# Performance work log

Measured on AMD Instinct MI355X. Metric: run time of the kernel, lower is better.

The kernel has to match this reference:

```python
import jax, jax.numpy as jnp
import numpy as np

HIDDEN = 1024
OUT = 8192
N_SUBJ = 8
B = 64
T = 512


def setup_inputs() -> dict:
    key = jax.random.key(0)
    ks = jax.random.split(key, 12)
    s = 1.0 / np.sqrt(HIDDEN)
    return {
        "context": jax.random.normal(ks[0], (B, T, HIDDEN), dtype=jnp.float32),
        "subject_ids": jax.random.randint(ks[1], (B,), 0, N_SUBJ),
        "eps": jax.random.normal(ks[2], (B, OUT), dtype=jnp.float32),
        # pool_proj: Linear(H,H) -> GELU -> Linear(H,H); weights stored (in,out)
        "w1": jax.random.normal(ks[3], (HIDDEN, HIDDEN), dtype=jnp.float32) * s,
        "b1": jax.random.normal(ks[4], (HIDDEN,), dtype=jnp.float32) * s,
        "w2": jax.random.normal(ks[5], (HIDDEN, HIDDEN), dtype=jnp.float32) * s,
        "b2": jax.random.normal(ks[6], (HIDDEN,), dtype=jnp.float32) * s,
        # SubjectLayers params, init normal(0, 1/sqrt(in))
        "subj_w": jax.random.normal(ks[7], (N_SUBJ, HIDDEN, OUT), dtype=jnp.float32) * s,
        "subj_b": jax.random.normal(ks[8], (N_SUBJ, OUT), dtype=jnp.float32) * s,
        # log_var head: weight std 1e-4, bias -2.0
        "lv_w": jax.random.normal(ks[9], (HIDDEN, OUT), dtype=jnp.float32) * 1e-4,
        "lv_b": jnp.full((OUT,), -2.0, dtype=jnp.float32),
    }


def reference(context, subject_ids, eps, w1, b1, w2, b2, subj_w, subj_b, lv_w, lv_b):
    # mean-pool over time: (B,T,H) -> (B,H)
    h = context.mean(axis=1)
    # pool_proj MLP with exact GELU (torch default)
    h = jax.nn.gelu(h @ w1 + b1, approximate=False) @ w2 + b2
    # per-subject linear head: gather (H,OUT) weight per sample, matvec
    w = subj_w[subject_ids]            # (B, H, OUT)
    mu = jnp.einsum("bd,bdo->bo", h, w) + subj_b[subject_ids]
    # variational log-variance head, clamped
    log_var = jnp.clip(h @ lv_w + lv_b, -10.0, 2.0)
    # reparameterized sample (training mode)
    x0 = mu + eps * jnp.exp(0.5 * log_var)
    return x0, mu, log_var
```

## Files before the change

kernel.cpp:

```cpp
#include <hip/hip_runtime.h>
#include <math.h>

#define HID   1024
#define OUTD  8192
#define NSUBJ 8
#define BATCH 64
#define TLEN  512

#define OFF_PP    0u
#define OFF_P1    1048576u
#define OFF_P2    3145728u
#define OFF_H     5242880u
#define OFF_MUP   5308416u
#define OFF_LVP   9502720u

__global__ __launch_bounds__(256) void k_pool(const float* __restrict__ ctx,
                                              float* __restrict__ pp) {
    int b  = blockIdx.x;
    int tc = blockIdx.y;
    int hid = threadIdx.x * 4;
    const float* base = ctx + ((size_t)b * TLEN + (size_t)tc * 32) * HID + hid;
    float4 acc = make_float4(0.f, 0.f, 0.f, 0.f);
#pragma unroll 8
    for (int t = 0; t < 32; ++t) {
        float4 v = *(const float4*)(base + (size_t)t * HID);
        acc.x += v.x; acc.y += v.y; acc.z += v.z; acc.w += v.w;
    }
    *(float4*)(pp + ((size_t)tc * BATCH + b) * HID + hid) = acc;
}

__global__ __launch_bounds__(256) void k_mlp1(const float* __restrict__ pp,
                                              const float* __restrict__ w1,
                                              float* __restrict__ p1) {
    __shared__ float xs[32][34];
    int j  = blockIdx.x * 256 + threadIdx.x;
    int k0 = blockIdx.y * 32;
    int b0 = blockIdx.z * 32;
    {
        int bb = threadIdx.x >> 3;
        int kk = (threadIdx.x & 7) * 4;
        float4 s = make_float4(0.f, 0.f, 0.f, 0.f);
#pragma unroll
        for (int tc = 0; tc < 16; ++tc) {
            float4 v = *(const float4*)(pp + (size_t)tc * 65536 + (b0 + bb) * 1024 + k0 + kk);
            s.x += v.x; s.y += v.y; s.z += v.z; s.w += v.w;
        }
        const float inv = 1.0f / 512.0f;
        xs[bb][kk]     = s.x * inv;
        xs[bb][kk + 1] = s.y * inv;
        xs[bb][kk + 2] = s.z * inv;
        xs[bb][kk + 3] = s.w * inv;
    }
    __syncthreads();
    float acc[32];
#pragma unroll
    for (int i = 0; i < 32; ++i) acc[i] = 0.f;
    for (int kk = 0; kk < 32; kk += 2) {
        float wa = w1[(size_t)(k0 + kk) * HID + j];
        float wb = w1[(size_t)(k0 + kk + 1) * HID + j];
#pragma unroll
        for (int i = 0; i < 32; ++i) {
            acc[i] = fmaf(xs[i][kk], wa, acc[i]);
            acc[i] = fmaf(xs[i][kk + 1], wb, acc[i]);
        }
    }
    float* dst = p1 + (size_t)blockIdx.y * 65536;
#pragma unroll
    for (int i = 0; i < 32; ++i) dst[(b0 + i) * 1024 + j] = acc[i];
}

__global__ __launch_bounds__(256) void k_mlp2(const float* __restrict__ p1,
                                              const float* __restrict__ b1,
                                              const float* __restrict__ w2,
                                              float* __restrict__ p2) {
    __shared__ float xs[32][34];
    int j  = blockIdx.x * 256 + threadIdx.x;
    int k0 = blockIdx.y * 32;
    int b0 = blockIdx.z * 32;
    {
        int bb = threadIdx.x >> 3;
        int kk = (threadIdx.x & 7) * 4;
        float4 s = make_float4(0.f, 0.f, 0.f, 0.f);
#pragma unroll
        for (int kc = 0; kc < 32; ++kc) {
            float4 v = *(const float4*)(p1 + (size_t)kc * 65536 + (b0 + bb) * 1024 + k0 + kk);
            s.x += v.x; s.y += v.y; s.z += v.z; s.w += v.w;
        }
        float4 bbv = *(const float4*)(b1 + k0 + kk);
        s.x += bbv.x; s.y += bbv.y; s.z += bbv.z; s.w += bbv.w;
        const float r = 0.70710678118654752f;
        xs[bb][kk]     = 0.5f * s.x * (1.0f + erff(s.x * r));
        xs[bb][kk + 1] = 0.5f * s.y * (1.0f + erff(s.y * r));
        xs[bb][kk + 2] = 0.5f * s.z * (1.0f + erff(s.z * r));
        xs[bb][kk + 3] = 0.5f * s.w * (1.0f + erff(s.w * r));
    }
    __syncthreads();
    float acc[32];
#pragma unroll
    for (int i = 0; i < 32; ++i) acc[i] = 0.f;
    for (int kk = 0; kk < 32; kk += 2) {
        float wa = w2[(size_t)(k0 + kk) * HID + j];
        float wb = w2[(size_t)(k0 + kk + 1) * HID + j];
#pragma unroll
        for (int i = 0; i < 32; ++i) {
            acc[i] = fmaf(xs[i][kk], wa, acc[i]);
            acc[i] = fmaf(xs[i][kk + 1], wb, acc[i]);
        }
    }
    float* dst = p2 + (size_t)blockIdx.y * 65536;
#pragma unroll
    for (int i = 0; i < 32; ++i) dst[(b0 + i) * 1024 + j] = acc[i];
}

__global__ __launch_bounds__(256) void k_red_bias(const float* __restrict__ p,
                                                  const float* __restrict__ bias,
                                                  float* __restrict__ out) {
    int i = (blockIdx.x * 256 + threadIdx.x) * 4;
    int j = i & (HID - 1);
    float4 s = make_float4(0.f, 0.f, 0.f, 0.f);
#pragma unroll
    for (int kc = 0; kc < 32; ++kc) {
        float4 v = *(const float4*)(p + (size_t)kc * 65536 + i);
        s.x += v.x; s.y += v.y; s.z += v.z; s.w += v.w;
    }
    float4 bb = *(const float4*)(bias + j);
    s.x += bb.x; s.y += bb.y; s.z += bb.z; s.w += bb.w;
    *(float4*)(out + i) = s;
}

template <int NS>
__device__ __forceinline__ void mu_tile(const float* __restrict__ hmat,
                                        const float* __restrict__ wbase,
                                        float* __restrict__ mup_kc,
                                        const int* bo, int n, int k0, int o) {
    float4 acc[NS];
#pragma unroll
    for (int i = 0; i < NS; ++i) acc[i] = make_float4(0.f, 0.f, 0.f, 0.f);
    float4 wv[4];
#pragma unroll
    for (int kk = 0; kk < 4; ++kk)
        wv[kk] = *(const float4*)(wbase + (size_t)(k0 + kk) * OUTD + o);
    for (int k = k0; k < k0 + 128; k += 4) {
        float4 hv[NS];
#pragma unroll
        for (int i = 0; i < NS; ++i)
            hv[i] = *(const float4*)(hmat + bo[i] * HID + k);
        int kn = (k + 4 < k0 + 128) ? (k + 4) : k0;
        float4 wn[4];
#pragma unroll
        for (int kk = 0; kk < 4; ++kk)
            wn[kk] = *(const float4*)(wbase + (size_t)(kn + kk) * OUTD + o);
#pragma unroll
        for (int kk = 0; kk < 4; ++kk) {
            float4 w = wv[kk];
#pragma unroll
            for (int i = 0; i < NS; ++i) {
                float h = (kk == 0) ? hv[i].x : (kk == 1) ? hv[i].y
                        : (kk == 2) ? hv[i].z : hv[i].w;
                acc[i].x = fmaf(h, w.x, acc[i].x);
                acc[i].y = fmaf(h, w.y, acc[i].y);
                acc[i].z = fmaf(h, w.z, acc[i].z);
                acc[i].w = fmaf(h, w.w, acc[i].w);
            }
        }
#pragma unroll
        for (int kk = 0; kk < 4; ++kk) wv[kk] = wn[kk];
    }
#pragma unroll
    for (int i = 0; i < NS; ++i)
        if (i < n) *(float4*)(mup_kc + (size_t)bo[i] * OUTD + o) = acc[i];
}

__global__ __launch_bounds__(256) void k_mu(const float* __restrict__ hmat,
                                            const float* __restrict__ subj_w,
                                            const int* __restrict__ sid,
                                            float* __restrict__ mup) {
    int o  = blockIdx.x * 1024 + threadIdx.x * 4;
    int k0 = blockIdx.y * 128;
    int s  = blockIdx.z;
    int lane = threadIdx.x & 63;
    int mysid = sid[lane];
    unsigned long long m = __ballot(mysid == s);
    int ns = __popcll(m);
    if (ns == 0) return;
    const float* wbase = subj_w + (size_t)s * HID * OUTD;
    float* mup_kc = mup + (size_t)blockIdx.y * BATCH * OUTD;
    unsigned long long mm = m;
    for (int base = 0; base < ns; base += 12) {
        int take = ns - base; if (take > 12) take = 12;
        int fb = (int)__builtin_ctzll(mm);
        int bo[12];
#pragma unroll
        for (int i = 0; i < 12; ++i) {
            bo[i] = (mm != 0ull) ? (int)__builtin_ctzll(mm) : fb;
            if (mm != 0ull) mm &= (mm - 1ull);
        }
        if (take <= 4)       mu_tile<4>(hmat, wbase, mup_kc, bo, take, k0, o);
        else if (take <= 8)  mu_tile<8>(hmat, wbase, mup_kc, bo, take, k0, o);
        else                 mu_tile<12>(hmat, wbase, mup_kc, bo, take, k0, o);
    }
}

__global__ __launch_bounds__(256) void k_lv(const float* __restrict__ hmat,
                                            const float* __restrict__ lv_w,
                                            float* __restrict__ lvp) {
    int o  = blockIdx.x * 512 + threadIdx.x * 2;
    int k0 = blockIdx.y * 128;
    int b0 = blockIdx.z * 32;
    float2 acc[32];
#pragma unroll
    for (int i = 0; i < 32; ++i) acc[i] = make_float2(0.f, 0.f);
    float2 wv0 = *(const float2*)(lv_w + (size_t)k0 * OUTD + o);
    float2 wv1 = *(const float2*)(lv_w + (size_t)(k0 + 1) * OUTD + o);
    for (int k = k0; k < k0 + 128; k += 2) {
        float2 hv[32];
#pragma unroll
        for (int i = 0; i < 32; ++i)
            hv[i] = *(const float2*)(hmat + (b0 + i) * HID + k);
        int kn = (k + 2 < k0 + 128) ? (k + 2) : k0;
        float2 wn0 = *(const float2*)(lv_w + (size_t)kn * OUTD + o);
        float2 wn1 = *(const float2*)(lv_w + (size_t)(kn + 1) * OUTD + o);
#pragma unroll
        for (int i = 0; i < 32; ++i) {
            acc[i].x = fmaf(hv[i].x, wv0.x, acc[i].x);
            acc[i].y = fmaf(hv[i].x, wv0.y, acc[i].y);
            acc[i].x = fmaf(hv[i].y, wv1.x, acc[i].x);
            acc[i].y = fmaf(hv[i].y, wv1.y, acc[i].y);
        }
        wv0 = wn0; wv1 = wn1;
    }
#pragma unroll
    for (int i = 0; i < 32; ++i) {
        float* dst = lvp + ((size_t)blockIdx.y * BATCH + b0 + i) * OUTD + o;
        dst[0] = acc[i].x; dst[1] = acc[i].y;
    }
}

__global__ __launch_bounds__(256) void k_combine(const float* __restrict__ mup,
                                                 const float* __restrict__ lvp,
                                                 const float* __restrict__ eps,
                                                 const float* __restrict__ subj_b,
                                                 const float* __restrict__ lv_b,
                                                 const int* __restrict__ sid,
                                                 float* __restrict__ out) {
    int idx = (blockIdx.x * 256 + threadIdx.x) * 4;
    int b = idx >> 13;
    int o = idx & (OUTD - 1);
    float4 m = make_float4(0.f, 0.f, 0.f, 0.f);
    float4 l = make_float4(0.f, 0.f, 0.f, 0.f);
#pragma unroll
    for (int kc = 0; kc < 8; ++kc) {
        float4 t = *(const float4*)(mup + (size_t)kc * 524288 + idx);
        m.x += t.x; m.y += t.y; m.z += t.z; m.w += t.w;
        float4 u = *(const float4*)(lvp + (size_t)kc * 524288 + idx);
        l.x += u.x; l.y += u.y; l.z += u.z; l.w += u.w;
    }
    int s = sid[b];
    float4 sb = *(const float4*)(subj_b + s * OUTD + o);
    float4 lb = *(const float4*)(lv_b + o);
    m.x += sb.x; m.y += sb.y; m.z += sb.z; m.w += sb.w;
    l.x = fminf(fmaxf(l.x + lb.x, -10.f), 2.f);
    l.y = fminf(fmaxf(l.y + lb.y, -10.f), 2.f);
    l.z = fminf(fmaxf(l.z + lb.z, -10.f), 2.f);
    l.w = fminf(fmaxf(l.w + lb.w, -10.f), 2.f);
    float4 e = *(const float4*)(eps + idx);
    float4 x0;
    x0.x = m.x + e.x * __expf(0.5f * l.x);
    x0.y = m.y + e.y * __expf(0.5f * l.y);
    x0.z = m.z + e.z * __expf(0.5f * l.z);
    x0.w = m.w + e.w * __expf(0.5f * l.w);
    *(float4*)(out + idx) = x0;
    *(float4*)(out + 524288 + idx) = m;
    *(float4*)(out + 1048576 + idx) = l;
}

extern "C" void kernel_launch(void* const* d_in, const int* in_sizes, int n_in,
                              void* d_out, int out_size, void* d_ws, size_t ws_size,
                              hipStream_t stream) {
    const float* ctx    = (const float*)d_in[0];
    const int*   sid    = (const int*)  d_in[1];
    const float* eps    = (const float*)d_in[2];
    const float* w1     = (const float*)d_in[3];
    const float* b1     = (const float*)d_in[4];
    const float* w2     = (const float*)d_in[5];
    const float* b2     = (const float*)d_in[6];
    const float* subj_w = (const float*)d_in[7];
    const float* subj_b = (const float*)d_in[8];
    const float* lv_w   = (const float*)d_in[9];
    const float* lv_b   = (const float*)d_in[10];
    float* out = (float*)d_out;

    float* ws   = (float*)d_ws;
    float* pp   = ws + OFF_PP;
    float* p1   = ws + OFF_P1;
    float* p2   = ws + OFF_P2;
    float* hbuf = ws + OFF_H;
    float* mup  = ws + OFF_MUP;
    float* lvp  = ws + OFF_LVP;

    k_pool<<<dim3(BATCH, 16), 256, 0, stream>>>(ctx, pp);
    k_mlp1<<<dim3(4, 32, 2), 256, 0, stream>>>(pp, w1, p1);
    k_mlp2<<<dim3(4, 32, 2), 256, 0, stream>>>(p1, b1, w2, p2);
    k_red_bias<<<64, 256, 0, stream>>>(p2, b2, hbuf);
    k_mu<<<dim3(8, 8, NSUBJ), 256, 0, stream>>>(hbuf, subj_w, sid, mup);
    k_lv<<<dim3(16, 8, 2), 256, 0, stream>>>(hbuf, lv_w, lvp);
    k_combine<<<512, 256, 0, stream>>>(mup, lvp, eps, subj_b, lv_b, sid, out);
}
```

Baseline: 184.6 us.

## Fuse all stages into one cooperative persistent kernel with grid syncs

New measurement: 556.7 us. 202% more time.

```diff
diff --git a/kernel.cpp b/kernel.cpp
--- a/kernel.cpp
+++ b/kernel.cpp
@@ -1,5 +1,8 @@
 #include <hip/hip_runtime.h>
+#include <hip/hip_cooperative_groups.h>
 #include <math.h>
+
+namespace cg = cooperative_groups;
 
 #define HID   1024
 #define OUTD  8192
@@ -9,10 +12,315 @@
 
 #define OFF_PP    0u
 #define OFF_P1    1048576u
-#define OFF_P2    3145728u
-#define OFF_H     5242880u
-#define OFF_MUP   5308416u
-#define OFF_LVP   9502720u
+#define OFF_P2    2097152u
+#define OFF_H     3145728u
+#define OFF_MUP   3211264u
+#define OFF_LVP   7405568u
+#define OFF_CNT   11599872u
+
+template <int NS>
+__device__ __forceinline__ void mu_tile(const float* __restrict__ hmat,
+                                        const float* __restrict__ wbase,
+                                        float* __restrict__ mup_kc,
+                                        const int* bo, int n, int k0, int o) {
+    float4 acc[NS];
+#pragma unroll
+    for (int i = 0; i < NS; ++i) acc[i] = make_float4(0.f, 0.f, 0.f, 0.f);
+    float4 wv[4];
+#pragma unroll
+    for (int kk = 0; kk < 4; ++kk)
+        wv[kk] = *(const float4*)(wbase + (size_t)(k0 + kk) * OUTD + o);
+    for (int k = k0; k < k0 + 128; k += 4) {
+        float4 hv[NS];
+#pragma unroll
+        for (int i = 0; i < NS; ++i)
+            hv[i] = *(const float4*)(hmat + bo[i] * HID + k);
+        int kn = (k + 4 < k0 + 128) ? (k + 4) : k0;
+        float4 wn[4];
+#pragma unroll
+        for (int kk = 0; kk < 4; ++kk)
+            wn[kk] = *(const float4*)(wbase + (size_t)(kn + kk) * OUTD + o);
+#pragma unroll
+        for (int kk = 0; kk < 4; ++kk) {
+            float4 w = wv[kk];
+#pragma unroll
+            for (int i = 0; i < NS; ++i) {
+                float h = (kk == 0) ? hv[i].x : (kk == 1) ? hv[i].y
+                        : (kk == 2) ? hv[i].z : hv[i].w;
+                acc[i].x = fmaf(h, w.x, acc[i].x);
+                acc[i].y = fmaf(h, w.y, acc[i].y);
+                acc[i].z = fmaf(h, w.z, acc[i].z);
+                acc[i].w = fmaf(h, w.w, acc[i].w);
+            }
+        }
+#pragma unroll
+        for (int kk = 0; kk < 4; ++kk) wv[kk] = wn[kk];
+    }
+#pragma unroll
+    for (int i = 0; i < NS; ++i)
+        if (i < n) *(float4*)(mup_kc + (size_t)bo[i] * OUTD + o) = acc[i];
+}
+
+__device__ __forceinline__ void mu_task(int t, const float* __restrict__ hbuf,
+                                        const float* __restrict__ subj_w,
+                                        const int* __restrict__ sid,
+                                        float* __restrict__ mup, int tid) {
+    int o  = (t >> 6) * 1024 + tid * 4;
+    int kc = (t >> 3) & 7;
+    int s  = t & 7;
+    int k0 = kc * 128;
+    int lane = tid & 63;
+    int mysid = sid[lane];
+    unsigned long long m = __ballot(mysid == s);
+    int ns = __popcll(m);
+    if (ns == 0) return;
+    const float* wbase = subj_w + (size_t)s * HID * OUTD;
+    float* mup_kc = mup + (size_t)kc * BATCH * OUTD;
+    unsigned long long mm = m;
+    for (int base = 0; base < ns; base += 12) {
+        int take = ns - base; if (take > 12) take = 12;
+        int fb = (int)__builtin_ctzll(mm);
+        int bo[12];
+#pragma unroll
+        for (int i = 0; i < 12; ++i) {
+            bo[i] = (mm != 0ull) ? (int)__builtin_ctzll(mm) : fb;
+            if (mm != 0ull) mm &= (mm - 1ull);
+        }
+        if (take <= 4)       mu_tile<4>(hbuf, wbase, mup_kc, bo, take, k0, o);
+        else if (take <= 8)  mu_tile<8>(hbuf, wbase, mup_kc, bo, take, k0, o);
+        else                 mu_tile<12>(hbuf, wbase, mup_kc, bo, take, k0, o);
+    }
+}
+
+__device__ __forceinline__ void lv_task(int u, const float* __restrict__ hbuf,
+                                        const float* __restrict__ lv_w,
+                                        float* __restrict__ lvp, int tid) {
+    int o  = (u & 15) * 512 + tid * 2;
+    int kc = (u >> 4) & 7;
+    int b0 = (u >> 7) * 32;
+    int k0 = kc * 128;
+    float2 acc[32];
+#pragma unroll
+    for (int i = 0; i < 32; ++i) acc[i] = make_float2(0.f, 0.f);
+    float2 wv0 = *(const float2*)(lv_w + (size_t)k0 * OUTD + o);
+    float2 wv1 = *(const float2*)(lv_w + (size_t)(k0 + 1) * OUTD + o);
+    for (int k = k0; k < k0 + 128; k += 2) {
+        float2 hv[32];
+#pragma unroll
+        for (int i = 0; i < 32; ++i)
+            hv[i] = *(const float2*)(hbuf + (b0 + i) * HID + k);
+        int kn = (k + 2 < k0 + 128) ? (k + 2) : k0;
+        float2 wn0 = *(const float2*)(lv_w + (size_t)kn * OUTD + o);
+        float2 wn1 = *(const float2*)(lv_w + (size_t)(kn + 1) * OUTD + o);
+#pragma unroll
+        for (int i = 0; i < 32; ++i) {
+            acc[i].x = fmaf(hv[i].x, wv0.x, acc[i].x);
+            acc[i].y = fmaf(hv[i].x, wv0.y, acc[i].y);
+            acc[i].x = fmaf(hv[i].y, wv1.x, acc[i].x);
+            acc[i].y = fmaf(hv[i].y, wv1.y, acc[i].y);
+        }
+        wv0 = wn0; wv1 = wn1;
+    }
+#pragma unroll
+    for (int i = 0; i < 32; ++i) {
+        float* dst = lvp + ((size_t)kc * BATCH + b0 + i) * OUTD + o;
+        dst[0] = acc[i].x; dst[1] = acc[i].y;
+    }
+}
+
+__global__ __launch_bounds__(256, 2) void k_fused(
+        const float* __restrict__ ctx, const int* __restrict__ sid,
+        const float* __restrict__ eps,
+        const float* __restrict__ w1, const float* __restrict__ b1,
+        const float* __restrict__ w2, const float* __restrict__ b2,
+        const float* __restrict__ subj_w, const float* __restrict__ subj_b,
+        const float* __restrict__ lv_w, const float* __restrict__ lv_b,
+        float* __restrict__ out, float* __restrict__ ws) {
+    cg::grid_group grid = cg::this_grid();
+    float* pp   = ws + OFF_PP;
+    float* p1   = ws + OFF_P1;
+    float* p2   = ws + OFF_P2;
+    float* hbuf = ws + OFF_H;
+    float* mup  = ws + OFF_MUP;
+    float* lvp  = ws + OFF_LVP;
+    int* counter = (int*)(ws + OFF_CNT);
+    const int bid = blockIdx.x;
+    const int nb  = gridDim.x;
+    const int tid = threadIdx.x;
+    __shared__ float xs[32][72];
+    __shared__ int task_s;
+
+    if (bid == 0 && tid == 0) *counter = 0;
+    for (int t = bid; t < 1024; t += nb) {
+        int b = t >> 4, tc = t & 15;
+        int hid = tid * 4;
+        const float* base = ctx + ((size_t)b * TLEN + (size_t)tc * 32) * HID + hid;
+        float4 acc = make_float4(0.f, 0.f, 0.f, 0.f);
+#pragma unroll 8
+        for (int tt = 0; tt < 32; ++tt) {
+            float4 v = *(const float4*)(base + (size_t)tt * HID);
+            acc.x += v.x; acc.y += v.y; acc.z += v.z; acc.w += v.w;
+        }
+        *(float4*)(pp + ((size_t)tc * BATCH + b) * HID + hid) = acc;
+    }
+    __threadfence();
+    grid.sync();
+
+    for (int t = bid; t < 128; t += nb) {
+        int j  = (t & 3) * 256 + tid;
+        int k0 = ((t >> 2) & 15) * 64;
+        int b0 = (t >> 6) * 32;
+        {
+            int bb = tid >> 3;
+            int kk8 = (tid & 7) * 8;
+            float4 s0 = make_float4(0.f, 0.f, 0.f, 0.f);
+            float4 s1 = make_float4(0.f, 0.f, 0.f, 0.f);
+#pragma unroll
+            for (int tc = 0; tc < 16; ++tc) {
+                const float* bp = pp + (size_t)tc * 65536 + (b0 + bb) * HID + k0 + kk8;
+                float4 v0 = *(const float4*)bp;
+                float4 v1 = *(const float4*)(bp + 4);
+                s0.x += v0.x; s0.y += v0.y; s0.z += v0.z; s0.w += v0.w;
+                s1.x += v1.x; s1.y += v1.y; s1.z += v1.z; s1.w += v1.w;
+            }
+            const float inv = 1.0f / 512.0f;
+            s0.x *= inv; s0.y *= inv; s0.z *= inv; s0.w *= inv;
+            s1.x *= inv; s1.y *= inv; s1.z *= inv; s1.w *= inv;
+            *(float4*)&xs[bb][kk8]     = s0;
+            *(float4*)&xs[bb][kk8 + 4] = s1;
+        }
+        __syncthreads();
+        float acc[32];
+#pragma unroll
+        for (int i = 0; i < 32; ++i) acc[i] = 0.f;
+        for (int kk = 0; kk < 64; kk += 2) {
+            float wa = w1[(size_t)(k0 + kk) * HID + j];
+            float wb = w1[(size_t)(k0 + kk + 1) * HID + j];
+#pragma unroll
+            for (int i = 0; i < 32; ++i) {
+                acc[i] = fmaf(xs[i][kk], wa, acc[i]);
+                acc[i] = fmaf(xs[i][kk + 1], wb, acc[i]);
+            }
+        }
+        float* dst = p1 + (size_t)((t >> 2) & 15) * 65536;
+#pragma unroll
+        for (int i = 0; i < 32; ++i) dst[(b0 + i) * HID + j] = acc[i];
+        __syncthreads();
+    }
+    __threadfence();
+    grid.sync();
+
+    for (int t = bid; t < 128; t += nb) {
+        int j  = (t & 3) * 256 + tid;
+        int k0 = ((t >> 2) & 15) * 64;
+        int b0 = (t >> 6) * 32;
+        {
+            int bb = tid >> 3;
+            int kk8 = (tid & 7) * 8;
+            float4 s0 = make_float4(0.f, 0.f, 0.f, 0.f);
+            float4 s1 = make_float4(0.f, 0.f, 0.f, 0.f);
+#pragma unroll
+            for (int kc = 0; kc < 16; ++kc) {
+                const float* bp = p1 + (size_t)kc * 65536 + (b0 + bb) * HID + k0 + kk8;
+                float4 v0 = *(const float4*)bp;
+                float4 v1 = *(const float4*)(bp + 4);
+                s0.x += v0.x; s0.y += v0.y; s0.z += v0.z; s0.w += v0.w;
+                s1.x += v1.x; s1.y += v1.y; s1.z += v1.z; s1.w += v1.w;
+            }
+            float4 bv0 = *(const float4*)(b1 + k0 + kk8);
+            float4 bv1 = *(const float4*)(b1 + k0 + kk8 + 4);
+            s0.x += bv0.x; s0.y += bv0.y; s0.z += bv0.z; s0.w += bv0.w;
+            s1.x += bv1.x; s1.y += bv1.y; s1.z += bv1.z; s1.w += bv1.w;
+            const float r = 0.70710678118654752f;
+            xs[bb][kk8]     = 0.5f * s0.x * (1.0f + erff(s0.x * r));
+            xs[bb][kk8 + 1] = 0.5f * s0.y * (1.0f + erff(s0.y * r));
+            xs[bb][kk8 + 2] = 0.5f * s0.z * (1.0f + erff(s0.z * r));
+            xs[bb][kk8 + 3] = 0.5f * s0.w * (1.0f + erff(s0.w * r));
+            xs[bb][kk8 + 4] = 0.5f * s1.x * (1.0f + erff(s1.x * r));
+            xs[bb][kk8 + 5] = 0.5f * s1.y * (1.0f + erff(s1.y * r));
+            xs[bb][kk8 + 6] = 0.5f * s1.z * (1.0f + erff(s1.z * r));
+            xs[bb][kk8 + 7] = 0.5f * s1.w * (1.0f + erff(s1.w * r));
+        }
+        __syncthreads();
+        float acc[32];
+#pragma unroll
+        for (int i = 0; i < 32; ++i) acc[i] = 0.f;
+        for (int kk = 0; kk < 64; kk += 2) {
+            float wa = w2[(size_t)(k0 + kk) * HID + j];
+            float wb = w2[(size_t)(k0 + kk + 1) * HID + j];
+#pragma unroll
+            for (int i = 0; i < 32; ++i) {
+                acc[i] = fmaf(xs[i][kk], wa, acc[i]);
+                acc[i] = fmaf(xs[i][kk + 1], wb, acc[i]);
+            }
+        }
+        float* dst = p2 + (size_t)((t >> 2) & 15) * 65536;
+#pragma unroll
+        for (int i = 0; i < 32; ++i) dst[(b0 + i) * HID + j] = acc[i];
+        __syncthreads();
+    }
+    __threadfence();
+    grid.sync();
+
+    for (int t = bid; t < 64; t += nb) {
+        int i = t * 1024 + tid * 4;
+        float4 s = make_float4(0.f, 0.f, 0.f, 0.f);
+#pragma unroll
+        for (int kc = 0; kc < 16; ++kc) {
+            float4 v = *(const float4*)(p2 + (size_t)kc * 65536 + i);
+            s.x += v.x; s.y += v.y; s.z += v.z; s.w += v.w;
+        }
+        float4 bb = *(const float4*)(b2 + tid * 4);
+        s.x += bb.x; s.y += bb.y; s.z += bb.z; s.w += bb.w;
+        *(float4*)(hbuf + i) = s;
+    }
+    __threadfence();
+    grid.sync();
+
+    for (;;) {
+        __syncthreads();
+        if (tid == 0) task_s = atomicAdd(counter, 1);
+        __syncthreads();
+        int t = task_s;
+        if (t >= 768) break;
+        if (t < 512) mu_task(t, hbuf, subj_w, sid, mup, tid);
+        else         lv_task(t - 512, hbuf, lv_w, lvp, tid);
+    }
+    __threadfence();
+    grid.sync();
+
+    for (int t = bid; t < 512; t += nb) {
+        int idx = t * 1024 + tid * 4;
+        int b = idx >> 13;
+        int o = idx & (OUTD - 1);
+        float4 m = make_float4(0.f, 0.f, 0.f, 0.f);
+        float4 l = make_float4(0.f, 0.f, 0.f, 0.f);
+#pragma unroll
+        for (int kc = 0; kc < 8; ++kc) {
+            float4 tv = *(const float4*)(mup + (size_t)kc * 524288 + idx);
+            m.x += tv.x; m.y += tv.y; m.z += tv.z; m.w += tv.w;
+            float4 u = *(const float4*)(lvp + (size_t)kc * 524288 + idx);
+            l.x += u.x; l.y += u.y; l.z += u.z; l.w += u.w;
+        }
+        int s = sid[b];
+        float4 sb = *(const float4*)(subj_b + s * OUTD + o);
+        float4 lb = *(const float4*)(lv_b + o);
+        m.x += sb.x; m.y += sb.y; m.z += sb.z; m.w += sb.w;
+        l.x = fminf(fmaxf(l.x + lb.x, -10.f), 2.f);
+        l.y = fminf(fmaxf(l.y + lb.y, -10.f), 2.f);
+        l.z = fminf(fmaxf(l.z + lb.z, -10.f), 2.f);
+        l.w = fminf(fmaxf(l.w + lb.w, -10.f), 2.f);
+        float4 e = *(const float4*)(eps + idx);
+        float4 x0;
+        x0.x = m.x + e.x * __expf(0.5f * l.x);
+        x0.y = m.y + e.y * __expf(0.5f * l.y);
+        x0.z = m.z + e.z * __expf(0.5f * l.z);
+        x0.w = m.w + e.w * __expf(0.5f * l.w);
+        *(float4*)(out + idx) = x0;
+        *(float4*)(out + 524288 + idx) = m;
+        *(float4*)(out + 1048576 + idx) = l;
+    }
+}
 
 __global__ __launch_bounds__(256) void k_pool(const float* __restrict__ ctx,
                                               float* __restrict__ pp) {
@@ -114,126 +422,36 @@
 
 __global__ __launch_bounds__(256) void k_red_bias(const float* __restrict__ p,
                                                   const float* __restrict__ bias,
-                                                  float* __restrict__ out) {
+                                                  float* __restrict__ out,
+                                                  int nchunk) {
     int i = (blockIdx.x * 256 + threadIdx.x) * 4;
     int j = i & (HID - 1);
     float4 s = make_float4(0.f, 0.f, 0.f, 0.f);
-#pragma unroll
-    for (int kc = 0; kc < 32; ++kc) {
+    for (int kc = 0; kc < nchunk; ++kc) {
         float4 v = *(const float4*)(p + (size_t)kc * 65536 + i);
         s.x += v.x; s.y += v.y; s.z += v.z; s.w += v.w;
     }
     float4 bb = *(const float4*)(bias + j);
     s.x += bb.x; s.y += bb.y; s.z += bb.z; s.w += bb.w;
     *(float4*)(out + i) = s;
-}
-
-template <int NS>
-__device__ __forceinline__ void mu_tile(const float* __restrict__ hmat,
-                                        const float* __restrict__ wbase,
-                                        float* __restrict__ mup_kc,
-                                        const int* bo, int n, int k0, int o) {
-    float4 acc[NS];
-#pragma unroll
-    for (int i = 0; i < NS; ++i) acc[i] = make_float4(0.f, 0.f, 0.f, 0.f);
-    float4 wv[4];
-#pragma unroll
-    for (int kk = 0; kk < 4; ++kk)
-        wv[kk] = *(const float4*)(wbase + (size_t)(k0 + kk) * OUTD + o);
-    for (int k = k0; k < k0 + 128; k += 4) {
-        float4 hv[NS];
-#pragma unroll
-        for (int i = 0; i < NS; ++i)
-            hv[i] = *(const float4*)(hmat + bo[i] * HID + k);
-        int kn = (k + 4 < k0 + 128) ? (k + 4) : k0;
-        float4 wn[4];
-#pragma unroll
-        for (int kk = 0; kk < 4; ++kk)
-            wn[kk] = *(const float4*)(wbase + (size_t)(kn + kk) * OUTD + o);
-#pragma unroll
-        for (int kk = 0; kk < 4; ++kk) {
-            float4 w = wv[kk];
-#pragma unroll
-            for (int i = 0; i < NS; ++i) {
-                float h = (kk == 0) ? hv[i].x : (kk == 1) ? hv[i].y
-                        : (kk == 2) ? hv[i].z : hv[i].w;
-                acc[i].x = fmaf(h, w.x, acc[i].x);
-                acc[i].y = fmaf(h, w.y, acc[i].y);
-                acc[i].z = fmaf(h, w.z, acc[i].z);
-                acc[i].w = fmaf(h, w.w, acc[i].w);
-            }
-        }
-#pragma unroll
-        for (int kk = 0; kk < 4; ++kk) wv[kk] = wn[kk];
-    }
-#pragma unroll
-    for (int i = 0; i < NS; ++i)
-        if (i < n) *(float4*)(mup_kc + (size_t)bo[i] * OUTD + o) = acc[i];
 }
 
 __global__ __launch_bounds__(256) void k_mu(const float* __restrict__ hmat,
                                             const float* __restrict__ subj_w,
                                             const int* __restrict__ sid,
                                             float* __restrict__ mup) {
-    int o  = blockIdx.x * 1024 + threadIdx.x * 4;
-    int k0 = blockIdx.y * 128;
-    int s  = blockIdx.z;
-    int lane = threadIdx.x & 63;
-    int mysid = sid[lane];
-    unsigned long long m = __ballot(mysid == s);
-    int ns = __popcll(m);
-    if (ns == 0) return;
-    const float* wbase = subj_w + (size_t)s * HID * OUTD;
-    float* mup_kc = mup + (size_t)blockIdx.y * BATCH * OUTD;
-    unsigned long long mm = m;
-    for (int base = 0; base < ns; base += 12) {
-        int take = ns - base; if (take > 12) take = 12;
-        int fb = (int)__builtin_ctzll(mm);
-        int bo[12];
-#pragma unroll
-        for (int i = 0; i < 12; ++i) {
-            bo[i] = (mm != 0ull) ? (int)__builtin_ctzll(mm) : fb;
-            if (mm != 0ull) mm &= (mm - 1ull);
-        }
-        if (take <= 4)       mu_tile<4>(hmat, wbase, mup_kc, bo, take, k0, o);
-        else if (take <= 8)  mu_tile<8>(hmat, wbase, mup_kc, bo, take, k0, o);
-        else                 mu_tile<12>(hmat, wbase, mup_kc, bo, take, k0, o);
-    }
+    int t = (blockIdx.z * 8 + blockIdx.y) * 8 + blockIdx.x;
+    (void)t;
+    int tid = threadIdx.x;
+    int task = ((blockIdx.x) << 6) + (blockIdx.y << 3) + blockIdx.z;
+    mu_task(task, hmat, subj_w, sid, mup, tid);
 }
 
 __global__ __launch_bounds__(256) void k_lv(const float* __restrict__ hmat,
                                             const float* __restrict__ lv_w,
                                             float* __restrict__ lvp) {
-    int o  = blockIdx.x * 512 + threadIdx.x * 2;
-    int k0 = blockIdx.y * 128;
-    int b0 = blockIdx.z * 32;
-    float2 acc[32];
-#pragma unroll
-    for (int i = 0; i < 32; ++i) acc[i] = make_float2(0.f, 0.f);
-    float2 wv0 = *(const float2*)(lv_w + (size_t)k0 * OUTD + o);
-    float2 wv1 = *(const float2*)(lv_w + (size_t)(k0 + 1) * OUTD + o);
-    for (int k = k0; k < k0 + 128; k += 2) {
-        float2 hv[32];
-#pragma unroll
-        for (int i = 0; i < 32; ++i)
-            hv[i] = *(const float2*)(hmat + (b0 + i) * HID + k);
-        int kn = (k + 2 < k0 + 128) ? (k + 2) : k0;
-        float2 wn0 = *(const float2*)(lv_w + (size_t)kn * OUTD + o);
-        float2 wn1 = *(const float2*)(lv_w + (size_t)(kn + 1) * OUTD + o);
-#pragma unroll
-        for (int i = 0; i < 32; ++i) {
-            acc[i].x = fmaf(hv[i].x, wv0.x, acc[i].x);
-            acc[i].y = fmaf(hv[i].x, wv0.y, acc[i].y);
-            acc[i].x = fmaf(hv[i].y, wv1.x, acc[i].x);
-            acc[i].y = fmaf(hv[i].y, wv1.y, acc[i].y);
-        }
-        wv0 = wn0; wv1 = wn1;
-    }
-#pragma unroll
-    for (int i = 0; i < 32; ++i) {
-        float* dst = lvp + ((size_t)blockIdx.y * BATCH + b0 + i) * OUTD + o;
-        dst[0] = acc[i].x; dst[1] = acc[i].y;
-    }
+    int u = (blockIdx.z << 7) + (blockIdx.y << 4) + blockIdx.x;
+    lv_task(u, hmat, lv_w, lvp, threadIdx.x);
 }
 
 __global__ __launch_bounds__(256) void k_combine(const float* __restrict__ mup,
@@ -289,8 +507,8 @@
     const float* lv_w   = (const float*)d_in[9];
     const float* lv_b   = (const float*)d_in[10];
     float* out = (float*)d_out;
-
-    float* ws   = (float*)d_ws;
+    float* ws  = (float*)d_ws;
+
     float* pp   = ws + OFF_PP;
     float* p1   = ws + OFF_P1;
     float* p2   = ws + OFF_P2;
@@ -298,10 +516,30 @@
     float* mup  = ws + OFF_MUP;
     float* lvp  = ws + OFF_LVP;
 
+    int dev = 0;
+    (void)hipGetDevice(&dev);
+    int coop = 0;
+    (void)hipDeviceGetAttribute(&coop, hipDeviceAttributeCooperativeLaunch, dev);
+    int occ = 0;
+    (void)hipOccupancyMaxActiveBlocksPerMultiprocessor(&occ, (const void*)k_fused, 256, 0);
+
+    if (coop && occ >= 1) {
+        int blocks = (occ >= 2) ? 512 : 256;
+        void* args[] = {
+            (void*)&ctx, (void*)&sid, (void*)&eps,
+            (void*)&w1, (void*)&b1, (void*)&w2, (void*)&b2,
+            (void*)&subj_w, (void*)&subj_b, (void*)&lv_w, (void*)&lv_b,
+            (void*)&out, (void*)&ws
+        };
+        hipError_t err = hipLaunchCooperativeKernel((const void*)k_fused, dim3(blocks),
+                                                    dim3(256), args, 0, stream);
+        if (err == hipSuccess) return;
+    }
+
     k_pool<<<dim3(BATCH, 16), 256, 0, stream>>>(ctx, pp);
     k_mlp1<<<dim3(4, 32, 2), 256, 0, stream>>>(pp, w1, p1);
     k_mlp2<<<dim3(4, 32, 2), 256, 0, stream>>>(p1, b1, w2, p2);
-    k_red_bias<<<64, 256, 0, stream>>>(p2, b2, hbuf);
+    k_red_bias<<<64, 256, 0, stream>>>(p2, b2, hbuf, 16);
     k_mu<<<dim3(8, 8, NSUBJ), 256, 0, stream>>>(hbuf, subj_w, sid, mup);
     k_lv<<<dim3(16, 8, 2), 256, 0, stream>>>(hbuf, lv_w, lvp);
     k_combine<<<512, 256, 0, stream>>>(mup, lvp, eps, subj_b, lv_b, sid, out);
```

## Fuse mu and log-var heads into one launch, split K finer for more blocks

Applied to the files above, without the earlier changes.

After: 207.8 us. +12.6%, slower.

```diff
diff --git a/kernel.cpp b/kernel.cpp
--- a/kernel.cpp
+++ b/kernel.cpp
@@ -8,21 +8,21 @@
 #define TLEN  512
 
 #define OFF_PP    0u
-#define OFF_P1    1048576u
-#define OFF_P2    3145728u
-#define OFF_H     5242880u
-#define OFF_MUP   5308416u
-#define OFF_LVP   9502720u
+#define OFF_P1    2097152u
+#define OFF_P2    4194304u
+#define OFF_H     6291456u
+#define OFF_MUP   6356992u
+#define OFF_LVP   14745600u
 
 __global__ __launch_bounds__(256) void k_pool(const float* __restrict__ ctx,
                                               float* __restrict__ pp) {
     int b  = blockIdx.x;
     int tc = blockIdx.y;
     int hid = threadIdx.x * 4;
-    const float* base = ctx + ((size_t)b * TLEN + (size_t)tc * 32) * HID + hid;
+    const float* base = ctx + ((size_t)b * TLEN + (size_t)tc * 16) * HID + hid;
     float4 acc = make_float4(0.f, 0.f, 0.f, 0.f);
-#pragma unroll 8
-    for (int t = 0; t < 32; ++t) {
+#pragma unroll
+    for (int t = 0; t < 16; ++t) {
         float4 v = *(const float4*)(base + (size_t)t * HID);
         acc.x += v.x; acc.y += v.y; acc.z += v.z; acc.w += v.w;
     }
@@ -41,7 +41,7 @@
         int kk = (threadIdx.x & 7) * 4;
         float4 s = make_float4(0.f, 0.f, 0.f, 0.f);
 #pragma unroll
-        for (int tc = 0; tc < 16; ++tc) {
+        for (int tc = 0; tc < 32; ++tc) {
             float4 v = *(const float4*)(pp + (size_t)tc * 65536 + (b0 + bb) * 1024 + k0 + kk);
             s.x += v.x; s.y += v.y; s.z += v.z; s.w += v.w;
         }
@@ -140,12 +140,12 @@
 #pragma unroll
     for (int kk = 0; kk < 4; ++kk)
         wv[kk] = *(const float4*)(wbase + (size_t)(k0 + kk) * OUTD + o);
-    for (int k = k0; k < k0 + 128; k += 4) {
+    for (int k = k0; k < k0 + 64; k += 4) {
         float4 hv[NS];
 #pragma unroll
         for (int i = 0; i < NS; ++i)
             hv[i] = *(const float4*)(hmat + bo[i] * HID + k);
-        int kn = (k + 4 < k0 + 128) ? (k + 4) : k0;
+        int kn = (k + 4 < k0 + 64) ? (k + 4) : k0;
         float4 wn[4];
 #pragma unroll
         for (int kk = 0; kk < 4; ++kk)
@@ -171,68 +171,73 @@
         if (i < n) *(float4*)(mup_kc + (size_t)bo[i] * OUTD + o) = acc[i];
 }
 
-__global__ __launch_bounds__(256) void k_mu(const float* __restrict__ hmat,
-                                            const float* __restrict__ subj_w,
-                                            const int* __restrict__ sid,
-                                            float* __restrict__ mup) {
-    int o  = blockIdx.x * 1024 + threadIdx.x * 4;
-    int k0 = blockIdx.y * 128;
-    int s  = blockIdx.z;
-    int lane = threadIdx.x & 63;
-    int mysid = sid[lane];
-    unsigned long long m = __ballot(mysid == s);
-    int ns = __popcll(m);
-    if (ns == 0) return;
-    const float* wbase = subj_w + (size_t)s * HID * OUTD;
-    float* mup_kc = mup + (size_t)blockIdx.y * BATCH * OUTD;
-    unsigned long long mm = m;
-    for (int base = 0; base < ns; base += 12) {
-        int take = ns - base; if (take > 12) take = 12;
-        int fb = (int)__builtin_ctzll(mm);
-        int bo[12];
-#pragma unroll
-        for (int i = 0; i < 12; ++i) {
-            bo[i] = (mm != 0ull) ? (int)__builtin_ctzll(mm) : fb;
-            if (mm != 0ull) mm &= (mm - 1ull);
-        }
-        if (take <= 4)       mu_tile<4>(hmat, wbase, mup_kc, bo, take, k0, o);
-        else if (take <= 8)  mu_tile<8>(hmat, wbase, mup_kc, bo, take, k0, o);
-        else                 mu_tile<12>(hmat, wbase, mup_kc, bo, take, k0, o);
-    }
-}
-
-__global__ __launch_bounds__(256) void k_lv(const float* __restrict__ hmat,
-                                            const float* __restrict__ lv_w,
-                                            float* __restrict__ lvp) {
-    int o  = blockIdx.x * 512 + threadIdx.x * 2;
-    int k0 = blockIdx.y * 128;
-    int b0 = blockIdx.z * 32;
-    float2 acc[32];
-#pragma unroll
-    for (int i = 0; i < 32; ++i) acc[i] = make_float2(0.f, 0.f);
-    float2 wv0 = *(const float2*)(lv_w + (size_t)k0 * OUTD + o);
-    float2 wv1 = *(const float2*)(lv_w + (size_t)(k0 + 1) * OUTD + o);
-    for (int k = k0; k < k0 + 128; k += 2) {
-        float2 hv[32];
-#pragma unroll
-        for (int i = 0; i < 32; ++i)
-            hv[i] = *(const float2*)(hmat + (b0 + i) * HID + k);
-        int kn = (k + 2 < k0 + 128) ? (k + 2) : k0;
-        float2 wn0 = *(const float2*)(lv_w + (size_t)kn * OUTD + o);
-        float2 wn1 = *(const float2*)(lv_w + (size_t)(kn + 1) * OUTD + o);
+__global__ __launch_bounds__(256) void k_head(const float* __restrict__ hbuf,
+                                              const float* __restrict__ subj_w,
+                                              const float* __restrict__ lv_w,
+                                              const int* __restrict__ sid,
+                                              float* __restrict__ mup,
+                                              float* __restrict__ lvp) {
+    int blk = blockIdx.x;
+    int tid = threadIdx.x;
+    if (blk < 1024) {
+        int o  = (blk >> 7) * 1024 + tid * 4;
+        int kc = (blk >> 3) & 15;
+        int s  = blk & 7;
+        int k0 = kc * 64;
+        int lane = tid & 63;
+        int mysid = sid[lane];
+        unsigned long long m = __ballot(mysid == s);
+        int ns = __popcll(m);
+        if (ns == 0) return;
+        const float* wbase = subj_w + (size_t)s * HID * OUTD;
+        float* mup_kc = mup + (size_t)kc * BATCH * OUTD;
+        unsigned long long mm = m;
+        for (int base = 0; base < ns; base += 12) {
+            int take = ns - base; if (take > 12) take = 12;
+            int fb = (int)__builtin_ctzll(mm);
+            int bo[12];
+#pragma unroll
+            for (int i = 0; i < 12; ++i) {
+                bo[i] = (mm != 0ull) ? (int)__builtin_ctzll(mm) : fb;
+                if (mm != 0ull) mm &= (mm - 1ull);
+            }
+            if (take <= 4)       mu_tile<4>(hbuf, wbase, mup_kc, bo, take, k0, o);
+            else if (take <= 8)  mu_tile<8>(hbuf, wbase, mup_kc, bo, take, k0, o);
+            else                 mu_tile<12>(hbuf, wbase, mup_kc, bo, take, k0, o);
+        }
+    } else {
+        int u  = blk - 1024;
+        int o  = (u & 15) * 512 + tid * 2;
+        int kc = (u >> 4) & 7;
+        int b0 = (u >> 7) * 32;
+        int k0 = kc * 128;
+        float2 acc[32];
+#pragma unroll
+        for (int i = 0; i < 32; ++i) acc[i] = make_float2(0.f, 0.f);
+        float2 wv0 = *(const float2*)(lv_w + (size_t)k0 * OUTD + o);
+        float2 wv1 = *(const float2*)(lv_w + (size_t)(k0 + 1) * OUTD + o);
+        for (int k = k0; k < k0 + 128; k += 2) {
+            float2 hv[32];
+#pragma unroll
+            for (int i = 0; i < 32; ++i)
+                hv[i] = *(const float2*)(hbuf + (b0 + i) * HID + k);
+            int kn = (k + 2 < k0 + 128) ? (k + 2) : k0;
+            float2 wn0 = *(const float2*)(lv_w + (size_t)kn * OUTD + o);
+            float2 wn1 = *(const float2*)(lv_w + (size_t)(kn + 1) * OUTD + o);
+#pragma unroll
+            for (int i = 0; i < 32; ++i) {
+                acc[i].x = fmaf(hv[i].x, wv0.x, acc[i].x);
+                acc[i].y = fmaf(hv[i].x, wv0.y, acc[i].y);
+                acc[i].x = fmaf(hv[i].y, wv1.x, acc[i].x);
+                acc[i].y = fmaf(hv[i].y, wv1.y, acc[i].y);
+            }
+            wv0 = wn0; wv1 = wn1;
+        }
 #pragma unroll
         for (int i = 0; i < 32; ++i) {
-            acc[i].x = fmaf(hv[i].x, wv0.x, acc[i].x);
-            acc[i].y = fmaf(hv[i].x, wv0.y, acc[i].y);
-            acc[i].x = fmaf(hv[i].y, wv1.x, acc[i].x);
-            acc[i].y = fmaf(hv[i].y, wv1.y, acc[i].y);
-        }
-        wv0 = wn0; wv1 = wn1;
-    }
-#pragma unroll
-    for (int i = 0; i < 32; ++i) {
-        float* dst = lvp + ((size_t)blockIdx.y * BATCH + b0 + i) * OUTD + o;
-        dst[0] = acc[i].x; dst[1] = acc[i].y;
+            float* dst = lvp + ((size_t)kc * BATCH + b0 + i) * OUTD + o;
+            dst[0] = acc[i].x; dst[1] = acc[i].y;
+        }
     }
 }
 
@@ -249,9 +254,12 @@
     float4 m = make_float4(0.f, 0.f, 0.f, 0.f);
     float4 l = make_float4(0.f, 0.f, 0.f, 0.f);
 #pragma unroll
-    for (int kc = 0; kc < 8; ++kc) {
+    for (int kc = 0; kc < 16; ++kc) {
         float4 t = *(const float4*)(mup + (size_t)kc * 524288 + idx);
         m.x += t.x; m.y += t.y; m.z += t.z; m.w += t.w;
+    }
+#pragma unroll
+    for (int kc = 0; kc < 8; ++kc) {
         float4 u = *(const float4*)(lvp + (size_t)kc * 524288 + idx);
         l.x += u.x; l.y += u.y; l.z += u.z; l.w += u.w;
     }
@@ -298,11 +306,10 @@
     float* mup  = ws + OFF_MUP;
     float* lvp  = ws + OFF_LVP;
 
-    k_pool<<<dim3(BATCH, 16), 256, 0, stream>>>(ctx, pp);
+    k_pool<<<dim3(BATCH, 32), 256, 0, stream>>>(ctx, pp);
     k_mlp1<<<dim3(4, 32, 2), 256, 0, stream>>>(pp, w1, p1);
     k_mlp2<<<dim3(4, 32, 2), 256, 0, stream>>>(p1, b1, w2, p2);
     k_red_bias<<<64, 256, 0, stream>>>(p2, b2, hbuf);
-    k_mu<<<dim3(8, 8, NSUBJ), 256, 0, stream>>>(hbuf, subj_w, sid, mup);
-    k_lv<<<dim3(16, 8, 2), 256, 0, stream>>>(hbuf, lv_w, lvp);
+    k_head<<<1280, 256, 0, stream>>>(hbuf, subj_w, lv_w, sid, mup, lvp);
     k_combine<<<512, 256, 0, stream>>>(mup, lvp, eps, subj_b, lv_b, sid, out);
 }
```

## Retile log-var head GEMM with shared-memory h and finer K split

Applied to the files above, without the earlier changes.

Measured after the change: 177.8 us. 1.04x faster.

```diff
diff --git a/kernel.cpp b/kernel.cpp
--- a/kernel.cpp
+++ b/kernel.cpp
@@ -204,36 +204,42 @@
 __global__ __launch_bounds__(256) void k_lv(const float* __restrict__ hmat,
                                             const float* __restrict__ lv_w,
                                             float* __restrict__ lvp) {
-    int o  = blockIdx.x * 512 + threadIdx.x * 2;
-    int k0 = blockIdx.y * 128;
-    int b0 = blockIdx.z * 32;
-    float2 acc[32];
-#pragma unroll
-    for (int i = 0; i < 32; ++i) acc[i] = make_float2(0.f, 0.f);
-    float2 wv0 = *(const float2*)(lv_w + (size_t)k0 * OUTD + o);
-    float2 wv1 = *(const float2*)(lv_w + (size_t)(k0 + 1) * OUTD + o);
-    for (int k = k0; k < k0 + 128; k += 2) {
-        float2 hv[32];
-#pragma unroll
-        for (int i = 0; i < 32; ++i)
-            hv[i] = *(const float2*)(hmat + (b0 + i) * HID + k);
-        int kn = (k + 2 < k0 + 128) ? (k + 2) : k0;
-        float2 wn0 = *(const float2*)(lv_w + (size_t)kn * OUTD + o);
-        float2 wn1 = *(const float2*)(lv_w + (size_t)(kn + 1) * OUTD + o);
-#pragma unroll
-        for (int i = 0; i < 32; ++i) {
-            acc[i].x = fmaf(hv[i].x, wv0.x, acc[i].x);
-            acc[i].y = fmaf(hv[i].x, wv0.y, acc[i].y);
-            acc[i].x = fmaf(hv[i].y, wv1.x, acc[i].x);
-            acc[i].y = fmaf(hv[i].y, wv1.y, acc[i].y);
-        }
-        wv0 = wn0; wv1 = wn1;
-    }
-#pragma unroll
-    for (int i = 0; i < 32; ++i) {
-        float* dst = lvp + ((size_t)blockIdx.y * BATCH + b0 + i) * OUTD + o;
-        dst[0] = acc[i].x; dst[1] = acc[i].y;
-    }
+    __shared__ float hs[64][20];
+    int o  = blockIdx.x * 1024 + threadIdx.x * 4;
+    int k0 = blockIdx.y * 64;
+    int b0 = blockIdx.z * 16;
+    {
+        int k  = threadIdx.x & 63;
+        int s4 = threadIdx.x >> 6;
+#pragma unroll
+        for (int j = 0; j < 4; ++j)
+            hs[k][s4 * 4 + j] = hmat[(size_t)(b0 + s4 * 4 + j) * HID + k0 + k];
+    }
+    __syncthreads();
+    float4 acc[16];
+#pragma unroll
+    for (int i = 0; i < 16; ++i) acc[i] = make_float4(0.f, 0.f, 0.f, 0.f);
+    const float* wp = lv_w + (size_t)k0 * OUTD + o;
+#pragma unroll 4
+    for (int k = 0; k < 64; ++k) {
+        float4 w = *(const float4*)(wp + (size_t)k * OUTD);
+        float4 h0 = *(const float4*)&hs[k][0];
+        float4 h1 = *(const float4*)&hs[k][4];
+        float4 h2 = *(const float4*)&hs[k][8];
+        float4 h3 = *(const float4*)&hs[k][12];
+        float hv[16] = {h0.x, h0.y, h0.z, h0.w, h1.x, h1.y, h1.z, h1.w,
+                        h2.x, h2.y, h2.z, h2.w, h3.x, h3.y, h3.z, h3.w};
+#pragma unroll
+        for (int i = 0; i < 16; ++i) {
+            acc[i].x = fmaf(hv[i], w.x, acc[i].x);
+            acc[i].y = fmaf(hv[i], w.y, acc[i].y);
+            acc[i].z = fmaf(hv[i], w.z, acc[i].z);
+            acc[i].w = fmaf(hv[i], w.w, acc[i].w);
+        }
+    }
+#pragma unroll
+    for (int i = 0; i < 16; ++i)
+        *(float4*)(lvp + ((size_t)blockIdx.y * BATCH + b0 + i) * OUTD + o) = acc[i];
 }
 
 __global__ __launch_bounds__(256) void k_combine(const float* __restrict__ mup,
@@ -252,6 +258,9 @@
     for (int kc = 0; kc < 8; ++kc) {
         float4 t = *(const float4*)(mup + (size_t)kc * 524288 + idx);
         m.x += t.x; m.y += t.y; m.z += t.z; m.w += t.w;
+    }
+#pragma unroll
+    for (int kc = 0; kc < 16; ++kc) {
         float4 u = *(const float4*)(lvp + (size_t)kc * 524288 + idx);
         l.x += u.x; l.y += u.y; l.z += u.z; l.w += u.w;
     }
@@ -303,6 +312,6 @@
     k_mlp2<<<dim3(4, 32, 2), 256, 0, stream>>>(p1, b1, w2, p2);
     k_red_bias<<<64, 256, 0, stream>>>(p2, b2, hbuf);
     k_mu<<<dim3(8, 8, NSUBJ), 256, 0, stream>>>(hbuf, subj_w, sid, mup);
-    k_lv<<<dim3(16, 8, 2), 256, 0, stream>>>(hbuf, lv_w, lvp);
+    k_lv<<<dim3(8, 16, 4), 256, 0, stream>>>(hbuf, lv_w, lvp);
     k_combine<<<512, 256, 0, stream>>>(mup, lvp, eps, subj_b, lv_b, sid, out);
 }
```
